# Kernel tuning notes

Measured on AMD Instinct MI355X. Metric: run time of the kernel, lower is better.

The kernel has to match this reference:

```python
import jax, jax.numpy as jnp
import numpy as np

N = 4096      # mesh nodes (seq len)
D = 512       # input_dim_nodes / hidden_size
F = 512       # ffn_hidden_size (hidden_dim)
NH = 4        # num_attention_heads
HD = D // NH  # head dim = 128
L = 2         # processor_layers
EPS = 1e-5
SCALE = 1.0 / float(np.sqrt(HD))
NEG = -1e9


def setup_inputs() -> dict:
    key = jax.random.key(0)
    ks = jax.random.split(key, 16)
    nfeat = jax.random.normal(ks[0], (N, D), jnp.float32)
    # sparse graph adjacency mask: True = masked out (TE 'arbitrary' convention)
    mask = jax.random.uniform(ks[1], (N, N)) < 0.99
    idx = jnp.arange(N)
    mask = mask.at[idx, idx].set(False)  # keep self-edges unmasked
    s = 0.02
    p = lambda k, shape: jax.random.normal(k, shape, jnp.float32) * s
    return dict(
        nfeat=nfeat, mask=mask,
        ln1_g=jnp.ones((L, D), jnp.float32), ln1_b=jnp.zeros((L, D), jnp.float32),
        wq=p(ks[2], (L, D, D)), bq=p(ks[3], (L, D)),
        wk=p(ks[4], (L, D, D)), bk=p(ks[5], (L, D)),
        wv=p(ks[6], (L, D, D)), bv=p(ks[7], (L, D)),
        wo=p(ks[8], (L, D, D)), bo=p(ks[9], (L, D)),
        ln2_g=jnp.ones((L, D), jnp.float32), ln2_b=jnp.zeros((L, D), jnp.float32),
        fc1_w=p(ks[10], (L, F, D)), fc1_b=p(ks[11], (L, F)),
        fc2_w=p(ks[12], (L, D, F)), fc2_b=p(ks[13], (L, D)),
    )


def _ln(x, g, b):
    mu = x.mean(-1, keepdims=True)
    var = ((x - mu) ** 2).mean(-1, keepdims=True)
    return (x - mu) * jax.lax.rsqrt(var + EPS) * g + b


def reference(nfeat, mask, ln1_g, ln1_b, wq, bq, wk, bk, wv, bv, wo, bo,
              ln2_g, ln2_b, fc1_w, fc1_b, fc2_w, fc2_b):
    def layer(x, p):
        g1, b1, Wq, Bq, Wk, Bk, Wv, Bv, Wo, Bo, g2, b2, W1, B1, W2, B2 = p
        # --- pre-LN self-attention with arbitrary mask ---
        h = _ln(x, g1, b1)                                  # [N, D]
        q = (h @ Wq.T + Bq).reshape(N, NH, HD)
        k = (h @ Wk.T + Bk).reshape(N, NH, HD)
        v = (h @ Wv.T + Bv).reshape(N, NH, HD)
        scores = jnp.einsum('qhd,khd->hqk', q, k) * SCALE   # [NH, N, N]
        scores = jnp.where(mask[None], NEG, scores)
        attn = jax.nn.softmax(scores, axis=-1)
        o = jnp.einsum('hqk,khd->qhd', attn, v).reshape(N, D)
        x = x + o @ Wo.T + Bo
        # --- pre-LN MLP ---
        h2 = _ln(x, g2, b2)
        m = jax.nn.gelu(h2 @ W1.T + B1, approximate=False) @ W2.T + B2
        return x + m, None

    xs = (ln1_g, ln1_b, wq, bq, wk, bk, wv, bv, wo, bo,
          ln2_g, ln2_b, fc1_w, fc1_b, fc2_w, fc2_b)
    out, _ = jax.lax.scan(layer, nfeat, xs)
    return out
```

## Files before the change

kernel.cpp:

```cpp
#include <hip/hip_runtime.h>
#include <math.h>

#define NN 4096
#define DD 512
#define FF 512
#define CAP 256
#define SCALE 0.08838834764831845f

typedef unsigned short u16;
typedef unsigned char u8;
typedef __attribute__((ext_vector_type(8))) short short8;
typedef __attribute__((ext_vector_type(8))) unsigned short ushort8;
typedef __attribute__((ext_vector_type(4))) unsigned short ushort4v;
typedef __attribute__((ext_vector_type(4))) float floatx4;
typedef __attribute__((ext_vector_type(2))) float f32x2;
typedef _Float16 half8v __attribute__((ext_vector_type(8)));

__device__ __forceinline__ float bf2f(u16 u) {
    union { unsigned int i; float f; } x; x.i = ((unsigned int)u) << 16; return x.f;
}
__device__ __forceinline__ u16 f2bf(float f) {
    union { float f; unsigned int i; } x; x.f = f;
    unsigned int r = (x.i + 0x7FFFu + ((x.i >> 16) & 1u)) >> 16;
    return (u16)r;
}
__device__ __forceinline__ u16 f2h(float f) {
    _Float16 h = (_Float16)f;
    union { _Float16 h; u16 u; } x; x.h = h; return x.u;
}
__device__ __forceinline__ u8 f2fp8(float f) {
    union { _Float16 h; u16 u; } x;
    x.h = (_Float16)(f * 0.00390625f);
    u16 h = x.u;
    h = h + 0x3F + ((h >> 7) & 1);
    return (u8)(((h >> 8) & 0x80) | ((h >> 7) & 0x7f));
}
__device__ __forceinline__ float fp82f_sw(u8 b) {
    union { u16 u; _Float16 h; } x;
    x.u = (u16)(((u16)(b & 0x80) << 8) | ((u16)(b & 0x7f) << 7));
    return (float)x.h * 256.0f;
}
__device__ __forceinline__ void gld_lds16(const void* g, void* l) {
    __builtin_amdgcn_global_load_lds((const __attribute__((address_space(1))) void*)g,
                                     (__attribute__((address_space(3))) void*)l, 16, 0, 0);
}

__global__ void build_idx_kernel(const int* __restrict__ mask,
                                 int* __restrict__ idx, int* __restrict__ cnt) {
    int row = blockIdx.x;
    __shared__ int c;
    if (threadIdx.x == 0) c = 0;
    __syncthreads();
    const int4* mrow = (const int4*)(mask + (size_t)row * NN);
    for (int j4 = threadIdx.x; j4 < NN / 4; j4 += blockDim.x) {
        int4 m4 = mrow[j4];
        int base = j4 * 4;
        if (m4.x == 0) idx[row * CAP + atomicAdd(&c, 1)] = base;
        if (m4.y == 0) idx[row * CAP + atomicAdd(&c, 1)] = base + 1;
        if (m4.z == 0) idx[row * CAP + atomicAdd(&c, 1)] = base + 2;
        if (m4.w == 0) idx[row * CAP + atomicAdd(&c, 1)] = base + 3;
    }
    __syncthreads();
    if (threadIdx.x == 0) cnt[row] = (c < CAP) ? c : CAP;
}

struct W6 {
    const float* w[6];
    const float* bq; const float* bk; const float* bv;
};
__global__ void cast_weights(W6 wp, u16* __restrict__ dst, float* __restrict__ bcat) {
    int region = blockIdx.x >> 4;
    int layer = region / 6, mat = region - layer * 6;
    const float* src = wp.w[mat] + (size_t)layer * (DD * DD);
    u16* d = dst + (size_t)region * (DD * DD);
    int off = (blockIdx.x & 15) * 16384 + threadIdx.x * 4;
#pragma unroll
    for (int i = 0; i < 16; i++) {
        int e = off + i * 1024;
        float4 f = *(const float4*)&src[e];
        ushort4v u;
        u.x = f2bf(f.x); u.y = f2bf(f.y); u.z = f2bf(f.z); u.w = f2bf(f.w);
        *(ushort4v*)&d[e] = u;
    }
    if (blockIdx.x < 2) {
        int l = blockIdx.x;
        for (int it = 0; it < 6; it++) {
            int j = it * 256 + threadIdx.x;
            int m = j >> 9, col = j & 511;
            const float* bp = (m == 0) ? wp.bq : (m == 1) ? wp.bk : wp.bv;
            bcat[l * 1536 + j] = bp[l * DD + col];
        }
    }
}

__global__ void ln_kernel(const float* __restrict__ x, const float* __restrict__ g,
                          const float* __restrict__ b, u16* __restrict__ out) {
    int wave = threadIdx.x >> 6, lane = threadIdx.x & 63;
    int row = blockIdx.x * 4 + wave;
    const float* xr = x + (size_t)row * DD;
    float4 p0 = *(const float4*)&xr[lane * 8];
    float4 p1 = *(const float4*)&xr[lane * 8 + 4];
    float v[8] = {p0.x, p0.y, p0.z, p0.w, p1.x, p1.y, p1.z, p1.w};
    float s = 0.f;
#pragma unroll
    for (int i = 0; i < 8; i++) s += v[i];
#pragma unroll
    for (int off = 32; off; off >>= 1) s += __shfl_xor(s, off);
    float mu = s * (1.0f / DD);
    float vs = 0.f;
#pragma unroll
    for (int i = 0; i < 8; i++) { float d = v[i] - mu; vs += d * d; }
#pragma unroll
    for (int off = 32; off; off >>= 1) vs += __shfl_xor(vs, off);
    float r = rsqrtf(vs * (1.0f / DD) + 1e-5f);
    float4 g0 = *(const float4*)&g[lane * 8];
    float4 g1 = *(const float4*)&g[lane * 8 + 4];
    float4 b0 = *(const float4*)&b[lane * 8];
    float4 b1 = *(const float4*)&b[lane * 8 + 4];
    float ge[8] = {g0.x, g0.y, g0.z, g0.w, g1.x, g1.y, g1.z, g1.w};
    float be[8] = {b0.x, b0.y, b0.z, b0.w, b1.x, b1.y, b1.z, b1.w};
    ushort8 ov;
#pragma unroll
    for (int i = 0; i < 8; i++) ov[i] = f2bf((v[i] - mu) * r * ge[i] + be[i]);
    *(ushort8*)&out[(size_t)row * DD + lane * 8] = ov;
}


template <int MODE>
__launch_bounds__(256)
__global__ void gemm_bf16(const u16* __restrict__ A, const u16* __restrict__ B,
                          const float* __restrict__ bias, const float* __restrict__ resIn,
                          float* __restrict__ resOut, u16* __restrict__ outB,
                          int M, int Nout, int K) {
    __shared__ u16 As[64 * 64];
    __shared__ u16 Bs[64 * 64];
    const int m0 = blockIdx.y * 64, n0 = blockIdx.x * 64;
    const int t = threadIdx.x;
    const int wave = t >> 6, lane = t & 63;
    const int wm = (wave & 1) * 32, wn = (wave >> 1) * 32;
    const int sr = t >> 3;
    const int sc = ((((t & 7) - (t >> 3)) & 7)) * 8;
    const int fr = lane & 15, g0 = lane >> 4;

    floatx4 acc[2][2] = {};
    const u16* ag0 = A + (size_t)(m0 + sr) * K + sc;
    const u16* ag1 = A + (size_t)(m0 + 32 + sr) * K + sc;
    const u16* bg0 = B + (size_t)(n0 + sr) * K + sc;
    const u16* bg1 = B + (size_t)(n0 + 32 + sr) * K + sc;
    u16* as0 = As + t * 8;
    u16* as1 = As + 32 * 64 + t * 8;
    u16* bs0 = Bs + t * 8;
    u16* bs1 = Bs + 32 * 64 + t * 8;

    for (int k0 = 0; k0 < K; k0 += 64) {
        __syncthreads();
        gld_lds16(ag0 + k0, as0);
        gld_lds16(ag1 + k0, as1);
        gld_lds16(bg0 + k0, bs0);
        gld_lds16(bg1 + k0, bs1);
        __syncthreads();
#pragma unroll
        for (int h = 0; h < 2; h++) {
            const int fo = (((h << 2) + g0 + fr) & 7) << 3;
            short8 af[2], bf[2];
#pragma unroll
            for (int i = 0; i < 2; i++) af[i] = *(const short8*)&As[(wm + 16 * i + fr) * 64 + fo];
#pragma unroll
            for (int j = 0; j < 2; j++) bf[j] = *(const short8*)&Bs[(wn + 16 * j + fr) * 64 + fo];
#pragma unroll
            for (int i = 0; i < 2; i++)
#pragma unroll
                for (int j = 0; j < 2; j++)
                    acc[i][j] = __builtin_amdgcn_mfma_f32_16x16x32_bf16(af[i], bf[j], acc[i][j], 0, 0, 0);
        }
    }

    const int er = (lane >> 4) * 4, ec = lane & 15;
#pragma unroll
    for (int i = 0; i < 2; i++) {
#pragma unroll
        for (int j = 0; j < 2; j++) {
            int col = n0 + wn + 16 * j + ec;
            float bsv = bias[col];
#pragma unroll
            for (int r = 0; r < 4; r++) {
                int row = m0 + wm + 16 * i + er + r;
                float val = acc[i][j][r] + bsv;
                if (MODE == 1) val = 0.5f * val * (1.0f + erff(val * 0.70710678118654752f));
                if (MODE == 2) {
                    resOut[(size_t)row * Nout + col] = resIn[(size_t)row * Nout + col] + val;
                } else {
                    outB[(size_t)row * Nout + col] = f2bf(val);
                }
            }
        }
    }
}

__launch_bounds__(256)
__global__ void gemm_qkv(const u16* __restrict__ A, const u16* __restrict__ B,
                         const float* __restrict__ bias, u16* __restrict__ qOut,
                         u8* __restrict__ kv8) {
    __shared__ u16 As[128 * 64];
    __shared__ u16 Bs[64 * 64];
    const int m0 = blockIdx.y * 128, n0 = blockIdx.x * 64;
    const int t = threadIdx.x;
    const int wave = t >> 6, lane = t & 63;
    const int wm = (wave & 1) * 64, wn = (wave >> 1) * 32;
    const int sr = t >> 3;
    const int sc = ((((t & 7) - (t >> 3)) & 7)) * 8;
    const int fr = lane & 15, g0 = lane >> 4;

    floatx4 acc[4][2] = {};
    const u16* agp[4];
    u16* asp[4];
#pragma unroll
    for (int u = 0; u < 4; u++) {
        agp[u] = A + (size_t)(m0 + 32 * u + sr) * DD + sc;
        asp[u] = As + u * (32 * 64) + t * 8;
    }
    const u16* bg0 = B + (size_t)(n0 + sr) * DD + sc;
    const u16* bg1 = B + (size_t)(n0 + 32 + sr) * DD + sc;
    u16* bs0 = Bs + t * 8;
    u16* bs1 = Bs + 32 * 64 + t * 8;

    for (int k0 = 0; k0 < DD; k0 += 64) {
        __syncthreads();
#pragma unroll
        for (int u = 0; u < 4; u++) gld_lds16(agp[u] + k0, asp[u]);
        gld_lds16(bg0 + k0, bs0);
        gld_lds16(bg1 + k0, bs1);
        __syncthreads();
#pragma unroll
        for (int h = 0; h < 2; h++) {
            const int fo = (((h << 2) + g0 + fr) & 7) << 3;
            short8 af[4], bf[2];
#pragma unroll
            for (int i = 0; i < 4; i++) af[i] = *(const short8*)&As[(wm + 16 * i + fr) * 64 + fo];
#pragma unroll
            for (int j = 0; j < 2; j++) bf[j] = *(const short8*)&Bs[(wn + 16 * j + fr) * 64 + fo];
#pragma unroll
            for (int i = 0; i < 4; i++)
#pragma unroll
                for (int j = 0; j < 2; j++)
                    acc[i][j] = __builtin_amdgcn_mfma_f32_16x16x32_bf16(af[i], bf[j], acc[i][j], 0, 0, 0);
        }
    }

    const int er = (lane >> 4) * 4, ec = lane & 15;
    const int bx = blockIdx.x;
#pragma unroll
    for (int j = 0; j < 2; j++) {
        int col = n0 + wn + 16 * j + ec;
        float bsv = bias[col];
#pragma unroll
        for (int i = 0; i < 4; i++) {
#pragma unroll
            for (int r = 0; r < 4; r++) {
                int row = m0 + wm + 16 * i + er + r;
                float val = acc[i][j][r] + bsv;
                if (bx < 8) {
                    qOut[(size_t)row * 512 + col] = f2h(val);
                } else if (bx < 16) {
                    int cc = col - 512;
                    kv8[(size_t)row * 1024 + 16 * (cc >> 3) + (cc & 7)] = f2fp8(val);
                } else {
                    int cc = col - 1024;
                    kv8[(size_t)row * 1024 + 16 * (cc >> 3) + 8 + (cc & 7)] = f2fp8(val);
                }
            }
        }
    }
}

__global__ void sparse_attn(const u16* __restrict__ q, const u8* __restrict__ kv8,
                            const int* __restrict__ idx, const int* __restrict__ cnt,
                            u16* __restrict__ o) {
    int t = threadIdx.x;
    int wave = t >> 6, lane = t & 63;
    int qslot = wave >> 1, half = wave & 1;
    int qi = blockIdx.x * 4 + qslot;
    __shared__ float obuf[4][64][8];
    __shared__ float sbuf[4][64];
    __shared__ int sidx[4][CAP];

    int c = cnt[qi];
    const int* ir = idx + qi * CAP;
    for (int j = t & 127; j < c; j += 128) sidx[qslot][j] = ir[j];

    half8v qv = *(const half8v*)(q + (size_t)qi * 512 + lane * 8);
    float qf[8];
#pragma unroll
    for (int e = 0; e < 8; e++) qf[e] = (float)qv[e];
    __syncthreads();

    float sum = 0.f, oa[8] = {};
    int j = half;
    int4 kvp;
    if (j < c) kvp = *(const int4*)(kv8 + (size_t)sidx[qslot][j] * 1024 + lane * 16);
    while (j < c) {
        int jn = j + 2;
        int4 kvn;
        {
            int kjn = (jn < c) ? sidx[qslot][jn] : 0;
            kvn = *(const int4*)(kv8 + (size_t)kjn * 1024 + lane * 16);
        }
        float kd[8], vd[8];
#if __has_builtin(__builtin_amdgcn_cvt_pk_f32_fp8)
        {
            f32x2 p0 = __builtin_amdgcn_cvt_pk_f32_fp8(kvp.x, false);
            f32x2 p1 = __builtin_amdgcn_cvt_pk_f32_fp8(kvp.x, true);
            f32x2 p2 = __builtin_amdgcn_cvt_pk_f32_fp8(kvp.y, false);
            f32x2 p3 = __builtin_amdgcn_cvt_pk_f32_fp8(kvp.y, true);
            kd[0] = p0.x; kd[1] = p0.y; kd[2] = p1.x; kd[3] = p1.y;
            kd[4] = p2.x; kd[5] = p2.y; kd[6] = p3.x; kd[7] = p3.y;
            f32x2 p4 = __builtin_amdgcn_cvt_pk_f32_fp8(kvp.z, false);
            f32x2 p5 = __builtin_amdgcn_cvt_pk_f32_fp8(kvp.z, true);
            f32x2 p6 = __builtin_amdgcn_cvt_pk_f32_fp8(kvp.w, false);
            f32x2 p7 = __builtin_amdgcn_cvt_pk_f32_fp8(kvp.w, true);
            vd[0] = p4.x; vd[1] = p4.y; vd[2] = p5.x; vd[3] = p5.y;
            vd[4] = p6.x; vd[5] = p6.y; vd[6] = p7.x; vd[7] = p7.y;
        }
#else
        {
            const u8* bp = (const u8*)&kvp;
#pragma unroll
            for (int e = 0; e < 8; e++) { kd[e] = fp82f_sw(bp[e]); vd[e] = fp82f_sw(bp[8 + e]); }
        }
#endif
        float d = 0.f;
#pragma unroll
        for (int e = 0; e < 8; e++) d = fmaf(qf[e], kd[e], d);
        d += __shfl_xor(d, 1);
        d += __shfl_xor(d, 2);
        d += __shfl_xor(d, 4);
        d += __shfl_xor(d, 8);
        float p = __expf(d * SCALE);
        sum += p;
#pragma unroll
        for (int e = 0; e < 8; e++) oa[e] = fmaf(p, vd[e], oa[e]);
        kvp = kvn;
        j = jn;
    }

    if (half == 1) {
#pragma unroll
        for (int e = 0; e < 8; e++) obuf[qslot][lane][e] = oa[e];
        sbuf[qslot][lane] = sum;
    }
    __syncthreads();
    if (half == 0) {
        sum += sbuf[qslot][lane];
        float inv = 1.0f / sum;
        ushort8 ov;
#pragma unroll
        for (int e = 0; e < 8; e++) ov[e] = f2bf((oa[e] + obuf[qslot][lane][e]) * inv);
        *(ushort8*)(o + (size_t)qi * 512 + lane * 8) = ov;
    }
}

extern "C" void kernel_launch(void* const* d_in, const int* in_sizes, int n_in,
                              void* d_out, int out_size, void* d_ws, size_t ws_size,
                              hipStream_t stream) {
    const float* nfeat = (const float*)d_in[0];
    const int*   mask  = (const int*)d_in[1];
    const float* ln1_g = (const float*)d_in[2];
    const float* ln1_b = (const float*)d_in[3];
    const float* bo    = (const float*)d_in[11];
    const float* ln2_g = (const float*)d_in[12];
    const float* ln2_b = (const float*)d_in[13];
    const float* fc1_b = (const float*)d_in[15];
    const float* fc2_b = (const float*)d_in[17];

    const size_t ND = (size_t)NN * DD;
    float* x    = (float*)d_ws;
    u16*   h    = (u16*)(x + ND);
    u16*   q    = h + ND;
    u8*    kv8  = (u8*)(q + ND);
    u16*   o    = (u16*)(kv8 + (size_t)NN * 1024);
    u16*   m1   = o + ND;
    u16*   wc   = m1 + ND;
    float* bcat = (float*)(wc + (size_t)12 * DD * DD);
    int*   idx  = (int*)(bcat + 2 * 1536);
    int*   cnt  = idx + (size_t)NN * CAP;

    W6 w6;
    w6.w[0] = (const float*)d_in[4];  w6.w[1] = (const float*)d_in[6];
    w6.w[2] = (const float*)d_in[8];  w6.w[3] = (const float*)d_in[10];
    w6.w[4] = (const float*)d_in[14]; w6.w[5] = (const float*)d_in[16];
    w6.bq = (const float*)d_in[5]; w6.bk = (const float*)d_in[7]; w6.bv = (const float*)d_in[9];
    cast_weights<<<192, 256, 0, stream>>>(w6, wc, bcat);
    build_idx_kernel<<<NN, 256, 0, stream>>>(mask, idx, cnt);

    const size_t SS = (size_t)DD * DD;
    for (int l = 0; l < 2; l++) {
        size_t bOff = (size_t)l * DD;
        u16* wl = wc + (size_t)l * 6 * SS;
        const float* xin = (l == 0) ? nfeat : x;
        float* fc2_dst = (l == 1) ? (float*)d_out : x;

        ln_kernel<<<NN / 4, 256, 0, stream>>>(xin, ln1_g + bOff, ln1_b + bOff, h);
        gemm_qkv<<<dim3(24, 32), 256, 0, stream>>>(h, wl, bcat + l * 1536, q, kv8);
        sparse_attn<<<NN / 4, 512, 0, stream>>>(q, kv8, idx, cnt, o);
        gemm_bf16<2><<<dim3(8, 64), 256, 0, stream>>>(o, wl + 3 * SS, bo + bOff,
                                                      xin, x, nullptr, NN, DD, DD);
        ln_kernel<<<NN / 4, 256, 0, stream>>>(x, ln2_g + bOff, ln2_b + bOff, h);
        gemm_bf16<1><<<dim3(8, 64), 256, 0, stream>>>(h, wl + 4 * SS, fc1_b + bOff,
                                                      nullptr, nullptr, m1, NN, FF, DD);
        gemm_bf16<2><<<dim3(8, 64), 256, 0, stream>>>(m1, wl + 5 * SS, fc2_b + bOff,
                                                      x, fc2_dst, nullptr, NN, DD, FF);
    }
}
```

Baseline: 276.6 us.

## Double-buffer GEMM LDS tiles, deepen attention prefetch, merge setup kernels, fast GELU

The mask-index build and the weight cast are merged into one launch. Both GEMM kernels now double-buffer their LDS tiles so the next K-tile loads while the current one computes, removing one barrier per iteration. The residual is preloaded into registers before the K loop. The sparse attention loop prefetches two KV rows ahead instead of one, and exact erf GELU is replaced by an Abramowitz-Stegun polynomial approximation, which costs some accuracy and doubles GEMM LDS use.

```diff
diff --git a/kernel.cpp b/kernel.cpp
--- a/kernel.cpp
+++ b/kernel.cpp
@@ -45,30 +45,31 @@
                                      (__attribute__((address_space(3))) void*)l, 16, 0, 0);
 }
 
-__global__ void build_idx_kernel(const int* __restrict__ mask,
-                                 int* __restrict__ idx, int* __restrict__ cnt) {
-    int row = blockIdx.x;
-    __shared__ int c;
-    if (threadIdx.x == 0) c = 0;
-    __syncthreads();
-    const int4* mrow = (const int4*)(mask + (size_t)row * NN);
-    for (int j4 = threadIdx.x; j4 < NN / 4; j4 += blockDim.x) {
-        int4 m4 = mrow[j4];
-        int base = j4 * 4;
-        if (m4.x == 0) idx[row * CAP + atomicAdd(&c, 1)] = base;
-        if (m4.y == 0) idx[row * CAP + atomicAdd(&c, 1)] = base + 1;
-        if (m4.z == 0) idx[row * CAP + atomicAdd(&c, 1)] = base + 2;
-        if (m4.w == 0) idx[row * CAP + atomicAdd(&c, 1)] = base + 3;
-    }
-    __syncthreads();
-    if (threadIdx.x == 0) cnt[row] = (c < CAP) ? c : CAP;
-}
-
 struct W6 {
     const float* w[6];
     const float* bq; const float* bk; const float* bv;
 };
-__global__ void cast_weights(W6 wp, u16* __restrict__ dst, float* __restrict__ bcat) {
+__global__ void setup_kernel(W6 wp, u16* __restrict__ dst, float* __restrict__ bcat,
+                             const int* __restrict__ mask, int* __restrict__ idx,
+                             int* __restrict__ cnt) {
+    __shared__ int c;
+    if (blockIdx.x >= 192) {
+        int row = blockIdx.x - 192;
+        if (threadIdx.x == 0) c = 0;
+        __syncthreads();
+        const int4* mrow = (const int4*)(mask + (size_t)row * NN);
+        for (int j4 = threadIdx.x; j4 < NN / 4; j4 += blockDim.x) {
+            int4 m4 = mrow[j4];
+            int base = j4 * 4;
+            if (m4.x == 0) idx[row * CAP + atomicAdd(&c, 1)] = base;
+            if (m4.y == 0) idx[row * CAP + atomicAdd(&c, 1)] = base + 1;
+            if (m4.z == 0) idx[row * CAP + atomicAdd(&c, 1)] = base + 2;
+            if (m4.w == 0) idx[row * CAP + atomicAdd(&c, 1)] = base + 3;
+        }
+        __syncthreads();
+        if (threadIdx.x == 0) cnt[row] = (c < CAP) ? c : CAP;
+        return;
+    }
     int region = blockIdx.x >> 4;
     int layer = region / 6, mat = region - layer * 6;
     const float* src = wp.w[mat] + (size_t)layer * (DD * DD);
@@ -125,6 +126,19 @@
     *(ushort8*)&out[(size_t)row * DD + lane * 8] = ov;
 }
 
+__device__ __forceinline__ float gelu_fast(float val) {
+    float z = fabsf(val) * 0.70710678118654752f;
+    float tt = __builtin_amdgcn_rcpf(fmaf(0.3275911f, z, 1.0f));
+    float p = fmaf(1.061405429f, tt, -1.453152027f);
+    p = fmaf(p, tt, 1.421413741f);
+    p = fmaf(p, tt, -0.284496736f);
+    p = fmaf(p, tt, 0.254829592f);
+    p = p * tt * __expf(-z * z);
+    float er_ = 1.0f - p;
+    float sgn = (val < 0.f) ? -er_ : er_;
+    return val * 0.5f * (1.0f + sgn);
+}
+
 
 template <int MODE>
 __launch_bounds__(256)
@@ -132,8 +146,8 @@
                           const float* __restrict__ bias, const float* __restrict__ resIn,
                           float* __restrict__ resOut, u16* __restrict__ outB,
                           int M, int Nout, int K) {
-    __shared__ u16 As[64 * 64];
-    __shared__ u16 Bs[64 * 64];
+    __shared__ u16 As[2 * 64 * 64];
+    __shared__ u16 Bs[2 * 64 * 64];
     const int m0 = blockIdx.y * 64, n0 = blockIdx.x * 64;
     const int t = threadIdx.x;
     const int wave = t >> 6, lane = t & 63;
@@ -141,6 +155,7 @@
     const int sr = t >> 3;
     const int sc = ((((t & 7) - (t >> 3)) & 7)) * 8;
     const int fr = lane & 15, g0 = lane >> 4;
+    const int er = (lane >> 4) * 4, ec = lane & 15;
 
     floatx4 acc[2][2] = {};
     const u16* ag0 = A + (size_t)(m0 + sr) * K + sc;
@@ -152,30 +167,51 @@
     u16* bs0 = Bs + t * 8;
     u16* bs1 = Bs + 32 * 64 + t * 8;
 
-    for (int k0 = 0; k0 < K; k0 += 64) {
+    float rin[16];
+    if (MODE == 2) {
+#pragma unroll
+        for (int i = 0; i < 2; i++)
+#pragma unroll
+            for (int j = 0; j < 2; j++)
+#pragma unroll
+                for (int r = 0; r < 4; r++)
+                    rin[(i * 2 + j) * 4 + r] =
+                        resIn[(size_t)(m0 + wm + 16 * i + er + r) * Nout + (n0 + wn + 16 * j + ec)];
+    }
+
+    auto stage = [&](int buf, int k0) {
+        int o = buf * 4096;
+        gld_lds16(ag0 + k0, as0 + o);
+        gld_lds16(ag1 + k0, as1 + o);
+        gld_lds16(bg0 + k0, bs0 + o);
+        gld_lds16(bg1 + k0, bs1 + o);
+    };
+
+    const int NK = K >> 6;
+    stage(0, 0);
+    int cur = 0;
+    for (int kt = 0; kt < NK; kt++) {
         __syncthreads();
-        gld_lds16(ag0 + k0, as0);
-        gld_lds16(ag1 + k0, as1);
-        gld_lds16(bg0 + k0, bs0);
-        gld_lds16(bg1 + k0, bs1);
-        __syncthreads();
+        if (kt + 1 < NK) stage(cur ^ 1, (kt + 1) * 64);
+        const u16* Ab = As + cur * 4096;
+        const u16* Bb = Bs + cur * 4096;
 #pragma unroll
         for (int h = 0; h < 2; h++) {
             const int fo = (((h << 2) + g0 + fr) & 7) << 3;
             short8 af[2], bf[2];
 #pragma unroll
-            for (int i = 0; i < 2; i++) af[i] = *(const short8*)&As[(wm + 16 * i + fr) * 64 + fo];
-#pragma unroll
-            for (int j = 0; j < 2; j++) bf[j] = *(const short8*)&Bs[(wn + 16 * j + fr) * 64 + fo];
+            for (int i = 0; i < 2; i++) af[i] = *(const short8*)&Ab[(wm + 16 * i + fr) * 64 + fo];
+#pragma unroll
+            for (int j = 0; j < 2; j++) bf[j] = *(const short8*)&Bb[(wn + 16 * j + fr) * 64 + fo];
 #pragma unroll
             for (int i = 0; i < 2; i++)
 #pragma unroll
                 for (int j = 0; j < 2; j++)
                     acc[i][j] = __builtin_amdgcn_mfma_f32_16x16x32_bf16(af[i], bf[j], acc[i][j], 0, 0, 0);
         }
-    }
-
-    const int er = (lane >> 4) * 4, ec = lane & 15;
+        cur ^= 1;
+    }
+
 #pragma unroll
     for (int i = 0; i < 2; i++) {
 #pragma unroll
@@ -186,9 +222,9 @@
             for (int r = 0; r < 4; r++) {
                 int row = m0 + wm + 16 * i + er + r;
                 float val = acc[i][j][r] + bsv;
-                if (MODE == 1) val = 0.5f * val * (1.0f + erff(val * 0.70710678118654752f));
+                if (MODE == 1) val = gelu_fast(val);
                 if (MODE == 2) {
-                    resOut[(size_t)row * Nout + col] = resIn[(size_t)row * Nout + col] + val;
+                    resOut[(size_t)row * Nout + col] = rin[(i * 2 + j) * 4 + r] + val;
                 } else {
                     outB[(size_t)row * Nout + col] = f2bf(val);
                 }
@@ -201,8 +237,8 @@
 __global__ void gemm_qkv(const u16* __restrict__ A, const u16* __restrict__ B,
                          const float* __restrict__ bias, u16* __restrict__ qOut,
                          u8* __restrict__ kv8) {
-    __shared__ u16 As[128 * 64];
-    __shared__ u16 Bs[64 * 64];
+    __shared__ u16 As[2 * 128 * 64];
+    __shared__ u16 Bs[2 * 64 * 64];
     const int m0 = blockIdx.y * 128, n0 = blockIdx.x * 64;
     const int t = threadIdx.x;
     const int wave = t >> 6, lane = t & 63;
@@ -224,27 +260,36 @@
     u16* bs0 = Bs + t * 8;
     u16* bs1 = Bs + 32 * 64 + t * 8;
 
-    for (int k0 = 0; k0 < DD; k0 += 64) {
+    auto stage = [&](int buf, int k0) {
+        int oa = buf * 8192, ob = buf * 4096;
+#pragma unroll
+        for (int u = 0; u < 4; u++) gld_lds16(agp[u] + k0, asp[u] + oa);
+        gld_lds16(bg0 + k0, bs0 + ob);
+        gld_lds16(bg1 + k0, bs1 + ob);
+    };
+
+    stage(0, 0);
+    int cur = 0;
+    for (int kt = 0; kt < 8; kt++) {
         __syncthreads();
-#pragma unroll
-        for (int u = 0; u < 4; u++) gld_lds16(agp[u] + k0, asp[u]);
-        gld_lds16(bg0 + k0, bs0);
-        gld_lds16(bg1 + k0, bs1);
-        __syncthreads();
+        if (kt + 1 < 8) stage(cur ^ 1, (kt + 1) * 64);
+        const u16* Ab = As + cur * 8192;
+        const u16* Bb = Bs + cur * 4096;
 #pragma unroll
         for (int h = 0; h < 2; h++) {
             const int fo = (((h << 2) + g0 + fr) & 7) << 3;
             short8 af[4], bf[2];
 #pragma unroll
-            for (int i = 0; i < 4; i++) af[i] = *(const short8*)&As[(wm + 16 * i + fr) * 64 + fo];
-#pragma unroll
-            for (int j = 0; j < 2; j++) bf[j] = *(const short8*)&Bs[(wn + 16 * j + fr) * 64 + fo];
+            for (int i = 0; i < 4; i++) af[i] = *(const short8*)&Ab[(wm + 16 * i + fr) * 64 + fo];
+#pragma unroll
+            for (int j = 0; j < 2; j++) bf[j] = *(const short8*)&Bb[(wn + 16 * j + fr) * 64 + fo];
 #pragma unroll
             for (int i = 0; i < 4; i++)
 #pragma unroll
                 for (int j = 0; j < 2; j++)
                     acc[i][j] = __builtin_amdgcn_mfma_f32_16x16x32_bf16(af[i], bf[j], acc[i][j], 0, 0, 0);
         }
+        cur ^= 1;
     }
 
     const int er = (lane >> 4) * 4, ec = lane & 15;
@@ -296,34 +341,38 @@
 
     float sum = 0.f, oa[8] = {};
     int j = half;
-    int4 kvp;
-    if (j < c) kvp = *(const int4*)(kv8 + (size_t)sidx[qslot][j] * 1024 + lane * 16);
+    int4 kv0, kv1;
+    {
+        int k0i = (j < c) ? sidx[qslot][j] : 0;
+        int k1i = (j + 2 < c) ? sidx[qslot][j + 2] : 0;
+        kv0 = *(const int4*)(kv8 + (size_t)k0i * 1024 + lane * 16);
+        kv1 = *(const int4*)(kv8 + (size_t)k1i * 1024 + lane * 16);
+    }
     while (j < c) {
-        int jn = j + 2;
         int4 kvn;
         {
-            int kjn = (jn < c) ? sidx[qslot][jn] : 0;
+            int kjn = (j + 4 < c) ? sidx[qslot][j + 4] : 0;
             kvn = *(const int4*)(kv8 + (size_t)kjn * 1024 + lane * 16);
         }
         float kd[8], vd[8];
 #if __has_builtin(__builtin_amdgcn_cvt_pk_f32_fp8)
         {
-            f32x2 p0 = __builtin_amdgcn_cvt_pk_f32_fp8(kvp.x, false);
-            f32x2 p1 = __builtin_amdgcn_cvt_pk_f32_fp8(kvp.x, true);
-            f32x2 p2 = __builtin_amdgcn_cvt_pk_f32_fp8(kvp.y, false);
-            f32x2 p3 = __builtin_amdgcn_cvt_pk_f32_fp8(kvp.y, true);
+            f32x2 p0 = __builtin_amdgcn_cvt_pk_f32_fp8(kv0.x, false);
+            f32x2 p1 = __builtin_amdgcn_cvt_pk_f32_fp8(kv0.x, true);
+            f32x2 p2 = __builtin_amdgcn_cvt_pk_f32_fp8(kv0.y, false);
+            f32x2 p3 = __builtin_amdgcn_cvt_pk_f32_fp8(kv0.y, true);
             kd[0] = p0.x; kd[1] = p0.y; kd[2] = p1.x; kd[3] = p1.y;
             kd[4] = p2.x; kd[5] = p2.y; kd[6] = p3.x; kd[7] = p3.y;
-            f32x2 p4 = __builtin_amdgcn_cvt_pk_f32_fp8(kvp.z, false);
-            f32x2 p5 = __builtin_amdgcn_cvt_pk_f32_fp8(kvp.z, true);
-            f32x2 p6 = __builtin_amdgcn_cvt_pk_f32_fp8(kvp.w, false);
-            f32x2 p7 = __builtin_amdgcn_cvt_pk_f32_fp8(kvp.w, true);
+            f32x2 p4 = __builtin_amdgcn_cvt_pk_f32_fp8(kv0.z, false);
+            f32x2 p5 = __builtin_amdgcn_cvt_pk_f32_fp8(kv0.z, true);
+            f32x2 p6 = __builtin_amdgcn_cvt_pk_f32_fp8(kv0.w, false);
+            f32x2 p7 = __builtin_amdgcn_cvt_pk_f32_fp8(kv0.w, true);
             vd[0] = p4.x; vd[1] = p4.y; vd[2] = p5.x; vd[3] = p5.y;
             vd[4] = p6.x; vd[5] = p6.y; vd[6] = p7.x; vd[7] = p7.y;
         }
 #else
         {
-            const u8* bp = (const u8*)&kvp;
+            const u8* bp = (const u8*)&kv0;
 #pragma unroll
             for (int e = 0; e < 8; e++) { kd[e] = fp82f_sw(bp[e]); vd[e] = fp82f_sw(bp[8 + e]); }
         }
@@ -339,8 +388,9 @@
         sum += p;
 #pragma unroll
         for (int e = 0; e < 8; e++) oa[e] = fmaf(p, vd[e], oa[e]);
-        kvp = kvn;
-        j = jn;
+        kv0 = kv1;
+        kv1 = kvn;
+        j += 2;
     }
 
     if (half == 1) {
@@ -389,8 +439,7 @@
     w6.w[2] = (const float*)d_in[8];  w6.w[3] = (const float*)d_in[10];
     w6.w[4] = (const float*)d_in[14]; w6.w[5] = (const float*)d_in[16];
     w6.bq = (const float*)d_in[5]; w6.bk = (const float*)d_in[7]; w6.bv = (const float*)d_in[9];
-    cast_weights<<<192, 256, 0, stream>>>(w6, wc, bcat);
-    build_idx_kernel<<<NN, 256, 0, stream>>>(mask, idx, cnt);
+    setup_kernel<<<192 + NN, 256, 0, stream>>>(w6, wc, bcat, mask, idx, cnt);
 
     const size_t SS = (size_t)DD * DD;
     for (int l = 0; l < 2; l++) {
```

Result: no change. 281.4 us (+1.7%).
